# Optimization experiments

Hardware: AMD Instinct MI355X
Metric: run time of the kernel (lower is better)

Reference implementation:

```python
import jax, jax.numpy as jnp
from jax import lax
import numpy as np

D_STATE = 16
D_CONV = 4
GROUPS = 4
TOKEN = 8


def group_norm(x, w, b, groups, eps=1e-5):
    # x: [B, C, H, W]; torch GroupNorm semantics
    B, C, H, W = x.shape
    xg = x.reshape(B, groups, C // groups, H, W)
    mu = xg.mean(axis=(2, 3, 4), keepdims=True)
    var = ((xg - mu) ** 2).mean(axis=(2, 3, 4), keepdims=True)
    xg = (xg - mu) / jnp.sqrt(var + eps)
    return xg.reshape(B, C, H, W) * w[None, :, None, None] + b[None, :, None, None]


def mamba_fwd(x, in_w, conv_w, conv_b, xproj_w, dt_w, dt_b, A_log, D, out_w):
    # x: [B, L, d_model]. Faithful mamba_ssm Mamba forward (no biases on in/out proj).
    Bsz, L, _ = x.shape
    d_inner = in_w.shape[0] // 2
    dt_rank = dt_w.shape[1]
    xz = x @ in_w.T                                   # [B, L, 2*d_inner]
    xi, z = jnp.split(xz, 2, axis=-1)
    # causal depthwise conv1d (kernel D_CONV) + SiLU
    xc = lax.conv_general_dilated(
        xi.transpose(0, 2, 1), conv_w, window_strides=(1,),
        padding=[(D_CONV - 1, 0)], dimension_numbers=("NCH", "OIH", "NCH"),
        feature_group_count=d_inner)
    xc = jax.nn.silu(xc + conv_b[None, :, None]).transpose(0, 2, 1)  # [B, L, d_inner]
    xdb = xc @ xproj_w.T                               # [B, L, dt_rank + 2*d_state]
    dt, Bm, Cm = jnp.split(xdb, [dt_rank, dt_rank + D_STATE], axis=-1)
    dt = jax.nn.softplus(dt @ dt_w.T + dt_b)           # [B, L, d_inner]
    A = -jnp.exp(A_log)                                # [d_inner, d_state]
    dA = jnp.exp(dt[..., None] * A)                    # [B, L, d_inner, d_state]
    dBx = dt[..., None] * Bm[:, :, None, :] * xc[..., None]

    def step(h, inp):
        dA_t, dBx_t, C_t = inp                         # [B,di,ds],[B,di,ds],[B,ds]
        h = dA_t * h + dBx_t
        y = jnp.einsum('bds,bs->bd', h, C_t)
        return h, y

    h0 = jnp.zeros((Bsz, d_inner, D_STATE), dtype=x.dtype)
    _, ys = lax.scan(step, h0, (dA.transpose(1, 0, 2, 3),
                                dBx.transpose(1, 0, 2, 3),
                                Cm.transpose(1, 0, 2)))
    y = ys.transpose(1, 0, 2) + xc * D                 # skip term D*x
    y = y * jax.nn.silu(z)
    return y @ out_w.T


def setup_inputs() -> dict:
    key = jax.random.key(0)
    ks = iter(jax.random.split(key, 48))

    def rn(shape, s=0.02):
        return jax.random.normal(next(ks), shape, dtype=jnp.float32) * s

    B, C, H, W = 4, 64, 64, 64
    inp = {"x": jax.random.normal(next(ks), (B, C, H, W), dtype=jnp.float32)}

    def mamba_params(prefix, d_model):
        d_inner = 2 * d_model
        dt_rank = -(-d_model // 16)
        inp[prefix + "_in_w"] = rn((2 * d_inner, d_model))
        inp[prefix + "_conv_w"] = rn((d_inner, 1, D_CONV))
        inp[prefix + "_conv_b"] = rn((d_inner,))
        inp[prefix + "_xproj_w"] = rn((dt_rank + 2 * D_STATE, d_inner))
        inp[prefix + "_dt_w"] = rn((d_inner, dt_rank))
        inp[prefix + "_dt_b"] = rn((d_inner,)) + 0.5
        inp[prefix + "_A_log"] = jnp.log(jnp.tile(jnp.arange(1, D_STATE + 1, dtype=jnp.float32), (d_inner, 1)))
        inp[prefix + "_D"] = jnp.ones((d_inner,), jnp.float32)
        inp[prefix + "_out_w"] = rn((d_model, d_inner))

    mamba_params("spa", C)
    mamba_params("spe", -(-C // TOKEN))  # group_channel_num = ceil(64/8) = 8
    inp["spa_gn_w"] = jnp.ones((C,), jnp.float32)
    inp["spa_gn_b"] = jnp.zeros((C,), jnp.float32)
    inp["spe_gn_w"] = jnp.ones((C,), jnp.float32)
    inp["spe_gn_b"] = jnp.zeros((C,), jnp.float32)
    inp["att_w"] = jnp.full((2,), 0.5, jnp.float32)
    return inp


def reference(x,
              spa_in_w, spa_conv_w, spa_conv_b, spa_xproj_w, spa_dt_w, spa_dt_b,
              spa_A_log, spa_D, spa_out_w,
              spe_in_w, spe_conv_w, spe_conv_b, spe_xproj_w, spe_dt_w, spe_dt_b,
              spe_A_log, spe_D, spe_out_w,
              spa_gn_w, spa_gn_b, spe_gn_w, spe_gn_b, att_w):
    B, C, H, W = x.shape
    gcn = -(-C // TOKEN)  # C == TOKEN*gcn here, so no padding path is taken

    # --- SpaMamba: flatten all pixels into one sequence [1, B*H*W, C] ---
    xs = x.transpose(0, 2, 3, 1).reshape(1, -1, C)
    ys = mamba_fwd(xs, spa_in_w, spa_conv_w, spa_conv_b, spa_xproj_w,
                   spa_dt_w, spa_dt_b, spa_A_log, spa_D, spa_out_w)
    ys = ys.reshape(B, H, W, C).transpose(0, 3, 1, 2)
    spa = jax.nn.silu(group_norm(ys, spa_gn_w, spa_gn_b, GROUPS)) + x

    # --- SpeMamba: per-pixel spectral tokens [B*H*W, TOKEN, gcn] ---
    xe = x.transpose(0, 2, 3, 1).reshape(B * H * W, TOKEN, gcn)
    ye = mamba_fwd(xe, spe_in_w, spe_conv_w, spe_conv_b, spe_xproj_w,
                   spe_dt_w, spe_dt_b, spe_A_log, spe_D, spe_out_w)
    ye = ye.reshape(B, H, W, C).transpose(0, 3, 1, 2)
    spe = x + jax.nn.silu(group_norm(ye, spe_gn_w, spe_gn_b, GROUPS))

    w = jax.nn.softmax(att_w)
    return spa * w[0] + spe * w[1] + x
```

## Files before the change

kernel.cpp:

```cpp
#include <hip/hip_runtime.h>

__device__ __forceinline__ float siluf(float x){ return x / (1.f + __expf(-x)); }
__device__ __forceinline__ float softplusf(float x){
    return fmaxf(x, 0.f) + __logf(1.f + __expf(-fabsf(x)));
}
#if __has_builtin(__builtin_amdgcn_exp2f)
__device__ __forceinline__ float fexp2(float x){ return __builtin_amdgcn_exp2f(x); }
#else
__device__ __forceinline__ float fexp2(float x){ return exp2f(x); }
#endif

__global__ void __launch_bounds__(256) k_xpose(const float* __restrict__ x, float* __restrict__ xs){
    __shared__ float t[64][65];
    int blk = blockIdx.x;
    int b = blk >> 6;
    int hw0 = (blk & 63) << 6;
    int tid = threadIdx.x;
    if (blk == 0 && tid < 192) xs[tid] = 0.f;
    const float* xb = x + b*262144 + hw0;
    #pragma unroll
    for (int it = 0; it < 16; ++it){
        int idx = it*256 + tid;
        t[idx>>6][idx&63] = xb[(idx>>6)*4096 + (idx&63)];
    }
    __syncthreads();
    float* xsb = xs + 192 + (size_t)(b*4096 + hw0)*64;
    #pragma unroll
    for (int it = 0; it < 16; ++it){
        int idx = it*256 + tid;
        xsb[(idx>>6)*64 + (idx&63)] = t[idx&63][idx>>6];
    }
}

__global__ void __launch_bounds__(256) k_inproj_conv(const float* __restrict__ xs,
        const float* __restrict__ in_w, const float* __restrict__ cw, const float* __restrict__ cb,
        float* __restrict__ xc, float* __restrict__ zb){
    int tid = threadIdx.x;
    int l0 = blockIdx.x * 8;
    float wr[64];
    const float4* w4 = (const float4*)(in_w + tid*64);
    #pragma unroll
    for (int k = 0; k < 16; ++k){
        float4 v = w4[k];
        wr[4*k]=v.x; wr[4*k+1]=v.y; wr[4*k+2]=v.z; wr[4*k+3]=v.w;
    }
    if (tid < 128){
        float acc[11];
        #pragma unroll
        for (int r = 0; r < 11; ++r) acc[r] = 0.f;
        const float4* xr = ((const float4*)xs) + (size_t)l0*16;
        #pragma unroll
        for (int k = 0; k < 16; ++k){
            #pragma unroll
            for (int r = 0; r < 11; ++r){
                float4 v = xr[r*16 + k];
                acc[r] = fmaf(v.x, wr[4*k],   acc[r]);
                acc[r] = fmaf(v.y, wr[4*k+1], acc[r]);
                acc[r] = fmaf(v.z, wr[4*k+2], acc[r]);
                acc[r] = fmaf(v.w, wr[4*k+3], acc[r]);
            }
        }
        float cw0 = cw[tid*4+0], cw1 = cw[tid*4+1], cw2 = cw[tid*4+2], cw3 = cw[tid*4+3];
        float cbd = cb[tid];
        #pragma unroll
        for (int r = 0; r < 8; ++r){
            float a = fmaf(cw0, acc[r],   cbd);
            a = fmaf(cw1, acc[r+1], a);
            a = fmaf(cw2, acc[r+2], a);
            a = fmaf(cw3, acc[r+3], a);
            xc[(size_t)(l0+r)*128 + tid] = siluf(a);
        }
    } else {
        float acc[8];
        #pragma unroll
        for (int r = 0; r < 8; ++r) acc[r] = 0.f;
        const float4* xr = ((const float4*)(xs + 192)) + (size_t)l0*16;
        #pragma unroll
        for (int k = 0; k < 16; ++k){
            #pragma unroll
            for (int r = 0; r < 8; ++r){
                float4 v = xr[r*16 + k];
                acc[r] = fmaf(v.x, wr[4*k],   acc[r]);
                acc[r] = fmaf(v.y, wr[4*k+1], acc[r]);
                acc[r] = fmaf(v.z, wr[4*k+2], acc[r]);
                acc[r] = fmaf(v.w, wr[4*k+3], acc[r]);
            }
        }
        int dz = tid - 128;
        #pragma unroll
        for (int r = 0; r < 8; ++r) zb[(size_t)(l0+r)*128 + dz] = acc[r];
    }
}

__global__ void __launch_bounds__(256) k_scan_p1(const float* __restrict__ xc,
        const float* __restrict__ xpw, const float* __restrict__ dtw, const float* __restrict__ dtb,
        const float* __restrict__ A_log, float* __restrict__ Pb, float* __restrict__ Qb){
    __shared__ float sxc[32*128];
    __shared__ float sbm[32*16];
    __shared__ __align__(16) float dtr[32][4];
    const int tid = threadIdx.x;
    const int ch = blockIdx.x;
    {
        const float4* src = (const float4*)(xc + (size_t)ch*4096);
        float4* dst = (float4*)sxc;
        #pragma unroll
        for (int u = 0; u < 4; ++u) dst[u*256 + tid] = src[u*256 + tid];
    }
    __syncthreads();
    {
        int j = tid & 63, tg = tid >> 6;
        if (j < 20){
            const float4* w4  = (const float4*)(xpw + j*128);
            const float4* xc4 = (const float4*)sxc + tg*256;
            float acc[8];
            #pragma unroll
            for (int r = 0; r < 8; ++r) acc[r] = 0.f;
            #pragma unroll 8
            for (int k = 0; k < 32; ++k){
                float4 w = w4[k];
                #pragma unroll
                for (int r = 0; r < 8; ++r){
                    float4 v = xc4[r*32 + k];
                    acc[r] = fmaf(v.x, w.x, acc[r]);
                    acc[r] = fmaf(v.y, w.y, acc[r]);
                    acc[r] = fmaf(v.z, w.z, acc[r]);
                    acc[r] = fmaf(v.w, w.w, acc[r]);
                }
            }
            if (j < 4){
                #pragma unroll
                for (int r = 0; r < 8; ++r) dtr[tg*8+r][j] = acc[r];
            } else {
                #pragma unroll
                for (int r = 0; r < 8; ++r) sbm[(tg*8+r)*16 + (j-4)] = acc[r];
            }
        }
    }
    __syncthreads();
    const int d  = tid & 127;
    const int sh = tid >> 7;
    float A8[8];
    {
        const float4* al4 = (const float4*)(A_log + d*16 + sh*8);
        float4 v0 = al4[0], v1 = al4[1];
        A8[0]=-__expf(v0.x)*1.44269504f; A8[1]=-__expf(v0.y)*1.44269504f;
        A8[2]=-__expf(v0.z)*1.44269504f; A8[3]=-__expf(v0.w)*1.44269504f;
        A8[4]=-__expf(v1.x)*1.44269504f; A8[5]=-__expf(v1.y)*1.44269504f;
        A8[6]=-__expf(v1.z)*1.44269504f; A8[7]=-__expf(v1.w)*1.44269504f;
    }
    float4 dw = *(const float4*)(dtw + d*4);
    float dbd = dtb[d];
    float P[8], Q[8];
    #pragma unroll
    for (int s = 0; s < 8; ++s){ P[s] = 1.f; Q[s] = 0.f; }
    #pragma unroll 4
    for (int i = 0; i < 32; ++i){
        float4 dt4 = *(const float4*)dtr[i];
        float dv = dbd;
        dv = fmaf(dt4.x, dw.x, dv);
        dv = fmaf(dt4.y, dw.y, dv);
        dv = fmaf(dt4.z, dw.z, dv);
        dv = fmaf(dt4.w, dw.w, dv);
        float dt = softplusf(dv);
        float db = dt * sxc[i*128 + d];
        const float4* bmr = (const float4*)(sbm + i*16 + sh*8);
        float4 b0 = bmr[0], b1 = bmr[1];
        float bv[8] = {b0.x,b0.y,b0.z,b0.w,b1.x,b1.y,b1.z,b1.w};
        #pragma unroll
        for (int s = 0; s < 8; ++s){
            float a = fexp2(dt*A8[s]);
            P[s] *= a;
            Q[s] = fmaf(a, Q[s], db*bv[s]);
        }
    }
    float* Pp = Pb + (size_t)ch*2048 + d*16 + sh*8;
    float* Qp = Qb + (size_t)ch*2048 + d*16 + sh*8;
    ((float4*)Pp)[0] = make_float4(P[0],P[1],P[2],P[3]);
    ((float4*)Pp)[1] = make_float4(P[4],P[5],P[6],P[7]);
    ((float4*)Qp)[0] = make_float4(Q[0],Q[1],Q[2],Q[3]);
    ((float4*)Qp)[1] = make_float4(Q[4],Q[5],Q[6],Q[7]);
}

__global__ void __launch_bounds__(256) k_scan_p2a(const float* __restrict__ Pb,
        const float* __restrict__ Qb, float* __restrict__ Ps, float* __restrict__ Qs){
    int g = blockIdx.x*256 + threadIdx.x;
    int sup = g >> 11;
    int lane = g & 2047;
    float P = 1.f, Q = 0.f;
    for (int i = 0; i < 32; i += 8){
        float p[8], q[8];
        #pragma unroll
        for (int u = 0; u < 8; ++u){
            p[u] = Pb[(size_t)(sup*32+i+u)*2048 + lane];
            q[u] = Qb[(size_t)(sup*32+i+u)*2048 + lane];
        }
        #pragma unroll
        for (int u = 0; u < 8; ++u){
            P = p[u]*P;
            Q = fmaf(p[u], Q, q[u]);
        }
    }
    Ps[g] = P; Qs[g] = Q;
}

__global__ void __launch_bounds__(256) k_scan_p2c(const float* __restrict__ Pb,
        const float* __restrict__ Qb, const float* __restrict__ Ps,
        const float* __restrict__ Qs, float* __restrict__ Hs){
    int g = blockIdx.x*256 + threadIdx.x;
    int sup = g >> 11;
    int lane = g & 2047;
    float h = 0.f;
    for (int u = 0; u < sup; ++u){
        float p = Ps[u*2048 + lane];
        float q = Qs[u*2048 + lane];
        h = fmaf(p, h, q);
    }
    for (int i = 0; i < 32; i += 8){
        float p[8], q[8];
        #pragma unroll
        for (int u = 0; u < 8; ++u){
            p[u] = Pb[(size_t)(sup*32+i+u)*2048 + lane];
            q[u] = Qb[(size_t)(sup*32+i+u)*2048 + lane];
        }
        #pragma unroll
        for (int u = 0; u < 8; ++u){
            Hs[(size_t)(sup*32+i+u)*2048 + lane] = h;
            h = fmaf(p[u], h, q[u]);
        }
    }
}

__global__ void __launch_bounds__(256) k_scan_p3(const float* __restrict__ xc,
        const float* __restrict__ zb, const float* __restrict__ xpw, const float* __restrict__ dtw,
        const float* __restrict__ dtb, const float* __restrict__ A_log, const float* __restrict__ Dv,
        const float* __restrict__ Hs, float* __restrict__ yg){
    __shared__ float sxc[32*128];
    __shared__ float ypl[2][32*128];
    __shared__ float sbm[32*16];
    __shared__ float scm[32*16];
    __shared__ __align__(16) float dtr[32][4];
    const int tid = threadIdx.x;
    const int ch = blockIdx.x;
    {
        const float4* src = (const float4*)(xc + (size_t)ch*4096);
        float4* dst = (float4*)sxc;
        #pragma unroll
        for (int u = 0; u < 4; ++u) dst[u*256 + tid] = src[u*256 + tid];
    }
    __syncthreads();
    {
        int j = tid & 63, tg = tid >> 6;
        if (j < 36){
            const float4* w4  = (const float4*)(xpw + j*128);
            const float4* xc4 = (const float4*)sxc + tg*256;
            float acc[8];
            #pragma unroll
            for (int r = 0; r < 8; ++r) acc[r] = 0.f;
            #pragma unroll 8
            for (int k = 0; k < 32; ++k){
                float4 w = w4[k];
                #pragma unroll
                for (int r = 0; r < 8; ++r){
                    float4 v = xc4[r*32 + k];
                    acc[r] = fmaf(v.x, w.x, acc[r]);
                    acc[r] = fmaf(v.y, w.y, acc[r]);
                    acc[r] = fmaf(v.z, w.z, acc[r]);
                    acc[r] = fmaf(v.w, w.w, acc[r]);
                }
            }
            if (j < 4){
                #pragma unroll
                for (int r = 0; r < 8; ++r) dtr[tg*8+r][j] = acc[r];
            } else if (j < 20){
                #pragma unroll
                for (int r = 0; r < 8; ++r) sbm[(tg*8+r)*16 + (j-4)] = acc[r];
            } else {
                #pragma unroll
                for (int r = 0; r < 8; ++r) scm[(tg*8+r)*16 + (j-20)] = acc[r];
            }
        }
    }
    __syncthreads();
    const int d  = tid & 127;
    const int sh = tid >> 7;
    float A8[8], h[8];
    {
        const float4* al4 = (const float4*)(A_log + d*16 + sh*8);
        float4 v0 = al4[0], v1 = al4[1];
        A8[0]=-__expf(v0.x)*1.44269504f; A8[1]=-__expf(v0.y)*1.44269504f;
        A8[2]=-__expf(v0.z)*1.44269504f; A8[3]=-__expf(v0.w)*1.44269504f;
        A8[4]=-__expf(v1.x)*1.44269504f; A8[5]=-__expf(v1.y)*1.44269504f;
        A8[6]=-__expf(v1.z)*1.44269504f; A8[7]=-__expf(v1.w)*1.44269504f;
        const float4* h4 = (const float4*)(Hs + (size_t)ch*2048 + d*16 + sh*8);
        float4 h0 = h4[0], h1 = h4[1];
        h[0]=h0.x; h[1]=h0.y; h[2]=h0.z; h[3]=h0.w;
        h[4]=h1.x; h[5]=h1.y; h[6]=h1.z; h[7]=h1.w;
    }
    float4 dw = *(const float4*)(dtw + d*4);
    float dbd = dtb[d];
    #pragma unroll 4
    for (int i = 0; i < 32; ++i){
        float4 dt4 = *(const float4*)dtr[i];
        float dv = dbd;
        dv = fmaf(dt4.x, dw.x, dv);
        dv = fmaf(dt4.y, dw.y, dv);
        dv = fmaf(dt4.z, dw.z, dv);
        dv = fmaf(dt4.w, dw.w, dv);
        float dt = softplusf(dv);
        float db = dt * sxc[i*128 + d];
        const float4* bmr = (const float4*)(sbm + i*16 + sh*8);
        const float4* cmr = (const float4*)(scm + i*16 + sh*8);
        float4 b0 = bmr[0], b1 = bmr[1];
        float4 c0 = cmr[0], c1 = cmr[1];
        float bv[8] = {b0.x,b0.y,b0.z,b0.w,b1.x,b1.y,b1.z,b1.w};
        float cv[8] = {c0.x,c0.y,c0.z,c0.w,c1.x,c1.y,c1.z,c1.w};
        float yp = 0.f;
        #pragma unroll
        for (int s = 0; s < 8; ++s){
            float a = fexp2(dt*A8[s]);
            h[s] = fmaf(a, h[s], db*bv[s]);
            yp = fmaf(h[s], cv[s], yp);
        }
        ypl[sh][i*128 + d] = yp;
    }
    __syncthreads();
    #pragma unroll
    for (int it = 0; it < 16; ++it){
        int idx = it*256 + tid;
        int i = idx >> 7, dd = idx & 127;
        float yp = ypl[0][i*128+dd] + ypl[1][i*128+dd];
        float xcd = sxc[i*128+dd];
        float zv = zb[(size_t)ch*4096 + idx];
        yg[(size_t)ch*4096 + idx] = (yp + xcd*Dv[dd]) * siluf(zv);
    }
}

__global__ void __launch_bounds__(256) k_spa_outproj(const float* __restrict__ yg,
        const float* __restrict__ ow, float* __restrict__ ys, float* __restrict__ sp){
    __shared__ float part[16][64];
    __shared__ float pg[2][2][4];
    int tid = threadIdx.x;
    int c  = tid & 63;
    int kh = (tid >> 6) & 1;
    int rg = tid >> 7;
    int l0 = blockIdx.x*16 + rg*8;
    float wr[64];
    const float4* w4 = (const float4*)(ow + c*128 + kh*64);
    #pragma unroll
    for (int k = 0; k < 16; ++k){
        float4 v = w4[k];
        wr[4*k]=v.x; wr[4*k+1]=v.y; wr[4*k+2]=v.z; wr[4*k+3]=v.w;
    }
    float acc[8];
    #pragma unroll
    for (int r = 0; r < 8; ++r) acc[r] = 0.f;
    const float4* yr = (const float4*)(yg + (size_t)l0*128 + kh*64);
    #pragma unroll
    for (int k = 0; k < 16; ++k){
        #pragma unroll
        for (int r = 0; r < 8; ++r){
            float4 v = yr[r*32 + k];
            acc[r] = fmaf(v.x, wr[4*k],   acc[r]);
            acc[r] = fmaf(v.y, wr[4*k+1], acc[r]);
            acc[r] = fmaf(v.z, wr[4*k+2], acc[r]);
            acc[r] = fmaf(v.w, wr[4*k+3], acc[r]);
        }
    }
    if (kh == 1){
        #pragma unroll
        for (int r = 0; r < 8; ++r) part[rg*8+r][c] = acc[r];
    }
    __syncthreads();
    if (kh == 0){
        float s = 0.f, ss = 0.f;
        #pragma unroll
        for (int r = 0; r < 8; ++r){
            float v = acc[r] + part[rg*8+r][c];
            ys[(size_t)(l0+r)*64 + c] = v;
            s += v; ss += v*v;
        }
        s += __shfl_xor(s,1); ss += __shfl_xor(ss,1);
        s += __shfl_xor(s,2); ss += __shfl_xor(ss,2);
        s += __shfl_xor(s,4); ss += __shfl_xor(ss,4);
        s += __shfl_xor(s,8); ss += __shfl_xor(ss,8);
        if ((c & 15) == 0){ pg[0][rg][c>>4] = s; pg[1][rg][c>>4] = ss; }
    }
    __syncthreads();
    if (tid < 4){
        int b = blockIdx.x >> 8, blk = blockIdx.x & 255;
        float S  = pg[0][0][tid] + pg[0][1][tid];
        float SS = pg[1][0][tid] + pg[1][1][tid];
        float* dst = sp + (size_t)(((0*4 + b)*4 + tid)*256 + blk)*2;
        dst[0] = S; dst[1] = SS;
    }
}

__global__ void __launch_bounds__(256) k_spe(
        const float* __restrict__ x,
        const float* __restrict__ in_w, const float* __restrict__ cw, const float* __restrict__ cb,
        const float* __restrict__ xpw, const float* __restrict__ dtw, const float* __restrict__ dtb,
        const float* __restrict__ A_log, const float* __restrict__ Dv, const float* __restrict__ ow,
        float* __restrict__ ye, float* __restrict__ sp)
{
    __shared__ float xe[64][17];
    __shared__ float xcl[8][16][17];
    __shared__ float bml[8][16][17];
    __shared__ float cml[8][16][17];
    __shared__ float dtl[8][17];
    __shared__ float yl[8][16][17];
    __shared__ float spg[2][4][4];

    const int tid = threadIdx.x;
    const int pix = tid >> 4;
    const int d   = tid & 15;
    const int p0  = blockIdx.x * 16;
    const int b   = p0 >> 12;
    const int hw0 = p0 & 4095;

    const float* xb = x + b*262144 + hw0;
    #pragma unroll
    for (int it = 0; it < 4; ++it){
        int idx = it*256 + tid;
        xe[idx>>4][idx&15] = xb[(idx>>4)*4096 + (idx&15)];
    }
    __syncthreads();

    float wi[8], wz[8];
    #pragma unroll
    for (int g = 0; g < 8; ++g){ wi[g] = in_w[d*8+g]; wz[g] = in_w[(16+d)*8+g]; }
    float xi[8], zz[8];
    #pragma unroll
    for (int t = 0; t < 8; ++t){
        float ai = 0.f, az = 0.f;
        #pragma unroll
        for (int g = 0; g < 8; ++g){
            float v = xe[t*8+g][pix];
            ai = fmaf(v, wi[g], ai);
            az = fmaf(v, wz[g], az);
        }
        xi[t] = ai; zz[t] = az;
    }
    float c0 = cw[d*4+0], c1 = cw[d*4+1], c2 = cw[d*4+2], c3 = cw[d*4+3];
    float cbd = cb[d];
    float xcr[8];
    #pragma unroll
    for (int t = 0; t < 8; ++t){
        float a = fmaf(c3, xi[t], cbd);
        if (t >= 1) a = fmaf(c2, xi[t-1], a);
        if (t >= 2) a = fmaf(c1, xi[t-2], a);
        if (t >= 3) a = fmaf(c0, xi[t-3], a);
        xcr[t] = siluf(a);
        xcl[t][d][pix] = xcr[t];
    }
    __syncthreads();

    {
        const float* wr = xpw + d*16;
        #pragma unroll
        for (int t = 0; t < 8; ++t){
            float acc = 0.f;
            #pragma unroll
            for (int k = 0; k < 16; ++k) acc = fmaf(xcl[t][k][pix], wr[k], acc);
            if (d == 0) dtl[t][pix] = acc;
            else bml[t][d-1][pix] = acc;
        }
    }
    {
        const float* wr = xpw + (17+d)*16;
        #pragma unroll
        for (int t = 0; t < 8; ++t){
            float acc = 0.f;
            #pragma unroll
            for (int k = 0; k < 16; ++k) acc = fmaf(xcl[t][k][pix], wr[k], acc);
            cml[t][d][pix] = acc;
        }
    }
    if (d == 15){
        const float* wr = xpw + 16*16;
        #pragma unroll
        for (int t = 0; t < 8; ++t){
            float acc = 0.f;
            #pragma unroll
            for (int k = 0; k < 16; ++k) acc = fmaf(xcl[t][k][pix], wr[k], acc);
            bml[t][15][pix] = acc;
        }
    }
    __syncthreads();

    float A16[16];
    #pragma unroll
    for (int s = 0; s < 16; ++s) A16[s] = -__expf(A_log[d*16+s]) * 1.44269504f;
    float dwd = dtw[d], dbd = dtb[d], Dd = Dv[d];
    float h[16];
    #pragma unroll
    for (int s = 0; s < 16; ++s) h[s] = 0.f;
    #pragma unroll
    for (int t = 0; t < 8; ++t){
        float dtd = softplusf(fmaf(dtl[t][pix], dwd, dbd));
        float db = dtd * xcr[t];
        float yp = 0.f;
        #pragma unroll
        for (int s = 0; s < 16; ++s){
            float a = fexp2(dtd*A16[s]);
            h[s] = fmaf(a, h[s], db*bml[t][s][pix]);
            yp = fmaf(h[s], cml[t][s][pix], yp);
        }
        yl[t][d][pix] = (yp + xcr[t]*Dd) * siluf(zz[t]);
    }
    __syncthreads();

    int t = d >> 1, m0 = (d & 1)*4;
    float acc[4];
    #pragma unroll
    for (int mm = 0; mm < 4; ++mm){
        const float* wr = ow + (m0+mm)*16;
        float a = 0.f;
        #pragma unroll
        for (int k = 0; k < 16; ++k) a = fmaf(yl[t][k][pix], wr[k], a);
        acc[mm] = a;
    }
    float4 o; o.x=acc[0]; o.y=acc[1]; o.z=acc[2]; o.w=acc[3];
    *(float4*)(ye + (size_t)(p0+pix)*64 + t*8 + m0) = o;

    float s  = acc[0]+acc[1]+acc[2]+acc[3];
    float ss = acc[0]*acc[0]+acc[1]*acc[1]+acc[2]*acc[2]+acc[3]*acc[3];
    s += __shfl_xor(s,1);  ss += __shfl_xor(ss,1);
    s += __shfl_xor(s,2);  ss += __shfl_xor(ss,2);
    s += __shfl_xor(s,16); ss += __shfl_xor(ss,16);
    s += __shfl_xor(s,32); ss += __shfl_xor(ss,32);
    int lane = tid & 63, wv = tid >> 6;
    if ((lane & 51) == 0){ spg[0][wv][(lane>>2)&3] = s; spg[1][wv][(lane>>2)&3] = ss; }
    __syncthreads();
    if (tid < 4){
        int blk = blockIdx.x & 255;
        float S  = spg[0][0][tid]+spg[0][1][tid]+spg[0][2][tid]+spg[0][3][tid];
        float SS = spg[1][0][tid]+spg[1][1][tid]+spg[1][2][tid]+spg[1][3][tid];
        float* dst = sp + (size_t)(((1*4 + b)*4 + tid)*256 + blk)*2;
        dst[0] = S; dst[1] = SS;
    }
}

__global__ void __launch_bounds__(256) k_final(const float* __restrict__ x,
        const float* __restrict__ ys, const float* __restrict__ ye,
        const float* __restrict__ sp,
        const float* __restrict__ gsw, const float* __restrict__ gsb,
        const float* __restrict__ gew, const float* __restrict__ geb,
        const float* __restrict__ attw, float* __restrict__ out){
    __shared__ float st[16];
    __shared__ float tys[32][65];
    __shared__ float tye[32][65];
    int tid = threadIdx.x;
    int b   = blockIdx.x >> 7;
    int hw0 = (blockIdx.x & 127) << 5;
    {
        int combo = tid >> 5;
        int j = tid & 31;
        int t = combo >> 2, g = combo & 3;
        const float4* bp = (const float4*)(sp + (size_t)((t*4+b)*4 + g)*512 + j*16);
        float s = 0.f, ss = 0.f;
        #pragma unroll
        for (int k = 0; k < 4; ++k){ float4 v = bp[k]; s += v.x+v.z; ss += v.y+v.w; }
        s += __shfl_xor(s,1);  ss += __shfl_xor(ss,1);
        s += __shfl_xor(s,2);  ss += __shfl_xor(ss,2);
        s += __shfl_xor(s,4);  ss += __shfl_xor(ss,4);
        s += __shfl_xor(s,8);  ss += __shfl_xor(ss,8);
        s += __shfl_xor(s,16); ss += __shfl_xor(ss,16);
        if (j == 0){
            float m = s * (1.f/65536.f);
            float v = ss * (1.f/65536.f) - m*m;
            st[combo*2]   = m;
            st[combo*2+1] = rsqrtf(v + 1e-5f);
        }
    }
    const float* ysb = ys + ((size_t)(b*4096 + hw0))*64;
    const float* yeb = ye + ((size_t)(b*4096 + hw0))*64;
    #pragma unroll
    for (int it = 0; it < 8; ++it){
        int idx = it*256 + tid;
        tys[idx>>6][idx&63] = ysb[idx];
        tye[idx>>6][idx&63] = yeb[idx];
    }
    __syncthreads();
    float a0 = attw[0], a1 = attw[1];
    float mx = fmaxf(a0, a1);
    float e0 = __expf(a0-mx), e1 = __expf(a1-mx);
    float inv = 1.f/(e0+e1);
    float w0 = e0*inv, w1 = e1*inv;
    #pragma unroll
    for (int it = 0; it < 8; ++it){
        int idx = it*256 + tid;
        int c = idx >> 5, hwi = idx & 31;
        int g = c >> 4;
        size_t gx = ((size_t)(b*64 + c))*4096 + hw0 + hwi;
        float xv = x[gx];
        float ns = (tys[hwi][c] - st[g*2])     * st[g*2+1]     * gsw[c] + gsb[c];
        float ne = (tye[hwi][c] - st[8+g*2])   * st[8+g*2+1]   * gew[c] + geb[c];
        out[gx] = w0*(siluf(ns)+xv) + w1*(xv+siluf(ne)) + xv;
    }
}

#define OFF_XS 0u
#define OFF_XC 1048832u
#define OFF_Z  3145984u
#define OFF_PB 5243136u
#define OFF_QB 6291712u
#define OFF_YG 7340288u
#define OFF_HS 9437440u
#define OFF_PS 10486016u
#define OFF_QS 10518784u
#define OFF_SP 10551552u

extern "C" void kernel_launch(void* const* d_in, const int* in_sizes, int n_in,
                              void* d_out, int out_size, void* d_ws, size_t ws_size,
                              hipStream_t stream) {
    const float* x           = (const float*)d_in[0];
    const float* spa_in_w    = (const float*)d_in[1];
    const float* spa_conv_w  = (const float*)d_in[2];
    const float* spa_conv_b  = (const float*)d_in[3];
    const float* spa_xproj_w = (const float*)d_in[4];
    const float* spa_dt_w    = (const float*)d_in[5];
    const float* spa_dt_b    = (const float*)d_in[6];
    const float* spa_A_log   = (const float*)d_in[7];
    const float* spa_D       = (const float*)d_in[8];
    const float* spa_out_w   = (const float*)d_in[9];
    const float* spe_in_w    = (const float*)d_in[10];
    const float* spe_conv_w  = (const float*)d_in[11];
    const float* spe_conv_b  = (const float*)d_in[12];
    const float* spe_xproj_w = (const float*)d_in[13];
    const float* spe_dt_w    = (const float*)d_in[14];
    const float* spe_dt_b    = (const float*)d_in[15];
    const float* spe_A_log   = (const float*)d_in[16];
    const float* spe_D       = (const float*)d_in[17];
    const float* spe_out_w   = (const float*)d_in[18];
    const float* spa_gn_w    = (const float*)d_in[19];
    const float* spa_gn_b    = (const float*)d_in[20];
    const float* spe_gn_w    = (const float*)d_in[21];
    const float* spe_gn_b    = (const float*)d_in[22];
    const float* att_w       = (const float*)d_in[23];

    float* ws  = (float*)d_ws;
    float* xs  = ws + OFF_XS;
    float* xc  = ws + OFF_XC;
    float* zb  = ws + OFF_Z;
    float* Pb  = ws + OFF_PB;
    float* Qb  = ws + OFF_QB;
    float* yg  = ws + OFF_YG;
    float* Hs  = ws + OFF_HS;
    float* Ps  = ws + OFF_PS;
    float* Qs  = ws + OFF_QS;
    float* sp  = ws + OFF_SP;
    float* ysb = ws + OFF_XS;
    float* yeb = ws + OFF_Z;
    float* out = (float*)d_out;

    k_xpose      <<<256,  256, 0, stream>>>(x, xs);
    k_inproj_conv<<<2048, 256, 0, stream>>>(xs, spa_in_w, spa_conv_w, spa_conv_b, xc, zb);
    k_scan_p1    <<<512,  256, 0, stream>>>(xc, spa_xproj_w, spa_dt_w, spa_dt_b, spa_A_log, Pb, Qb);
    k_scan_p2a   <<<128,  256, 0, stream>>>(Pb, Qb, Ps, Qs);
    k_scan_p2c   <<<128,  256, 0, stream>>>(Pb, Qb, Ps, Qs, Hs);
    k_scan_p3    <<<512,  256, 0, stream>>>(xc, zb, spa_xproj_w, spa_dt_w, spa_dt_b,
                                            spa_A_log, spa_D, Hs, yg);
    k_spa_outproj<<<1024, 256, 0, stream>>>(yg, spa_out_w, ysb, sp);
    k_spe        <<<1024, 256, 0, stream>>>(x, spe_in_w, spe_conv_w, spe_conv_b, spe_xproj_w,
                                            spe_dt_w, spe_dt_b, spe_A_log, spe_D, spe_out_w,
                                            yeb, sp);
    k_final      <<<512,  256, 0, stream>>>(x, ysb, yeb, sp, spa_gn_w, spa_gn_b,
                                            spe_gn_w, spe_gn_b, att_w, out);
}
```

Baseline: 141.4 us.

## Fuse spa out-proj into scan p3 and co-schedule spectral Mamba with scan p1

The spectral Mamba branch now runs as extra blocks (512..1535) inside the spatial scan phase-1 kernel, so the two independent workloads share one launch and can fill the GPU together. The spatial output projection and its group-norm partial sums move into the tail of scan_p3, which reuses the gated y held in shared memory instead of writing yg to global memory and reading it back in a separate kernel. This removes two launches and one full intermediate round trip. In exchange the fused p1 kernel needs about 40 KB of shared memory per block and p3 carries more register pressure (a 64-float weight array plus 16 accumulators), which may lower occupancy. The workspace layout and the partial-sum indexing in k_final are adjusted to match.

After: 120.2 us. 1.18x faster.

```diff
diff --git a/kernel.cpp b/kernel.cpp
--- a/kernel.cpp
+++ b/kernel.cpp
@@ -92,93 +92,239 @@
     }
 }
 
-__global__ void __launch_bounds__(256) k_scan_p1(const float* __restrict__ xc,
-        const float* __restrict__ xpw, const float* __restrict__ dtw, const float* __restrict__ dtb,
-        const float* __restrict__ A_log, float* __restrict__ Pb, float* __restrict__ Qb){
-    __shared__ float sxc[32*128];
-    __shared__ float sbm[32*16];
-    __shared__ __align__(16) float dtr[32][4];
+__global__ void __launch_bounds__(256) k_p1_spe(
+        const float* __restrict__ xc, const float* __restrict__ xpw, const float* __restrict__ dtw,
+        const float* __restrict__ dtb, const float* __restrict__ A_log,
+        float* __restrict__ Pb, float* __restrict__ Qb,
+        const float* __restrict__ x,
+        const float* __restrict__ ein_w, const float* __restrict__ ecw, const float* __restrict__ ecb,
+        const float* __restrict__ expw, const float* __restrict__ edtw, const float* __restrict__ edtb,
+        const float* __restrict__ eA_log, const float* __restrict__ eDv, const float* __restrict__ eow,
+        float* __restrict__ ye, float* __restrict__ sp)
+{
+    __shared__ float smem[9960];
     const int tid = threadIdx.x;
-    const int ch = blockIdx.x;
-    {
-        const float4* src = (const float4*)(xc + (size_t)ch*4096);
-        float4* dst = (float4*)sxc;
-        #pragma unroll
-        for (int u = 0; u < 4; ++u) dst[u*256 + tid] = src[u*256 + tid];
-    }
-    __syncthreads();
-    {
-        int j = tid & 63, tg = tid >> 6;
-        if (j < 20){
-            const float4* w4  = (const float4*)(xpw + j*128);
-            const float4* xc4 = (const float4*)sxc + tg*256;
-            float acc[8];
-            #pragma unroll
-            for (int r = 0; r < 8; ++r) acc[r] = 0.f;
-            #pragma unroll 8
-            for (int k = 0; k < 32; ++k){
-                float4 w = w4[k];
-                #pragma unroll
-                for (int r = 0; r < 8; ++r){
-                    float4 v = xc4[r*32 + k];
-                    acc[r] = fmaf(v.x, w.x, acc[r]);
-                    acc[r] = fmaf(v.y, w.y, acc[r]);
-                    acc[r] = fmaf(v.z, w.z, acc[r]);
-                    acc[r] = fmaf(v.w, w.w, acc[r]);
+    if (blockIdx.x < 512){
+        float* sxc = smem;
+        float* sbm = smem + 4096;
+        float* dtr = smem + 4608;
+        const int ch = blockIdx.x;
+        {
+            const float4* src = (const float4*)(xc + (size_t)ch*4096);
+            float4* dst = (float4*)sxc;
+            #pragma unroll
+            for (int u = 0; u < 4; ++u) dst[u*256 + tid] = src[u*256 + tid];
+        }
+        __syncthreads();
+        {
+            int j = tid & 63, tg = tid >> 6;
+            if (j < 20){
+                const float4* w4  = (const float4*)(xpw + j*128);
+                const float4* xc4 = (const float4*)sxc + tg*256;
+                float acc[8];
+                #pragma unroll
+                for (int r = 0; r < 8; ++r) acc[r] = 0.f;
+                #pragma unroll 8
+                for (int k = 0; k < 32; ++k){
+                    float4 w = w4[k];
+                    #pragma unroll
+                    for (int r = 0; r < 8; ++r){
+                        float4 v = xc4[r*32 + k];
+                        acc[r] = fmaf(v.x, w.x, acc[r]);
+                        acc[r] = fmaf(v.y, w.y, acc[r]);
+                        acc[r] = fmaf(v.z, w.z, acc[r]);
+                        acc[r] = fmaf(v.w, w.w, acc[r]);
+                    }
                 }
-            }
-            if (j < 4){
-                #pragma unroll
-                for (int r = 0; r < 8; ++r) dtr[tg*8+r][j] = acc[r];
-            } else {
-                #pragma unroll
-                for (int r = 0; r < 8; ++r) sbm[(tg*8+r)*16 + (j-4)] = acc[r];
-            }
-        }
-    }
-    __syncthreads();
-    const int d  = tid & 127;
-    const int sh = tid >> 7;
-    float A8[8];
-    {
-        const float4* al4 = (const float4*)(A_log + d*16 + sh*8);
-        float4 v0 = al4[0], v1 = al4[1];
-        A8[0]=-__expf(v0.x)*1.44269504f; A8[1]=-__expf(v0.y)*1.44269504f;
-        A8[2]=-__expf(v0.z)*1.44269504f; A8[3]=-__expf(v0.w)*1.44269504f;
-        A8[4]=-__expf(v1.x)*1.44269504f; A8[5]=-__expf(v1.y)*1.44269504f;
-        A8[6]=-__expf(v1.z)*1.44269504f; A8[7]=-__expf(v1.w)*1.44269504f;
-    }
-    float4 dw = *(const float4*)(dtw + d*4);
-    float dbd = dtb[d];
-    float P[8], Q[8];
-    #pragma unroll
-    for (int s = 0; s < 8; ++s){ P[s] = 1.f; Q[s] = 0.f; }
-    #pragma unroll 4
-    for (int i = 0; i < 32; ++i){
-        float4 dt4 = *(const float4*)dtr[i];
-        float dv = dbd;
-        dv = fmaf(dt4.x, dw.x, dv);
-        dv = fmaf(dt4.y, dw.y, dv);
-        dv = fmaf(dt4.z, dw.z, dv);
-        dv = fmaf(dt4.w, dw.w, dv);
-        float dt = softplusf(dv);
-        float db = dt * sxc[i*128 + d];
-        const float4* bmr = (const float4*)(sbm + i*16 + sh*8);
-        float4 b0 = bmr[0], b1 = bmr[1];
-        float bv[8] = {b0.x,b0.y,b0.z,b0.w,b1.x,b1.y,b1.z,b1.w};
-        #pragma unroll
-        for (int s = 0; s < 8; ++s){
-            float a = fexp2(dt*A8[s]);
-            P[s] *= a;
-            Q[s] = fmaf(a, Q[s], db*bv[s]);
-        }
-    }
-    float* Pp = Pb + (size_t)ch*2048 + d*16 + sh*8;
-    float* Qp = Qb + (size_t)ch*2048 + d*16 + sh*8;
-    ((float4*)Pp)[0] = make_float4(P[0],P[1],P[2],P[3]);
-    ((float4*)Pp)[1] = make_float4(P[4],P[5],P[6],P[7]);
-    ((float4*)Qp)[0] = make_float4(Q[0],Q[1],Q[2],Q[3]);
-    ((float4*)Qp)[1] = make_float4(Q[4],Q[5],Q[6],Q[7]);
+                if (j < 4){
+                    #pragma unroll
+                    for (int r = 0; r < 8; ++r) dtr[(tg*8+r)*4 + j] = acc[r];
+                } else {
+                    #pragma unroll
+                    for (int r = 0; r < 8; ++r) sbm[(tg*8+r)*16 + (j-4)] = acc[r];
+                }
+            }
+        }
+        __syncthreads();
+        const int d  = tid & 127;
+        const int sh = tid >> 7;
+        float A8[8];
+        {
+            const float4* al4 = (const float4*)(A_log + d*16 + sh*8);
+            float4 v0 = al4[0], v1 = al4[1];
+            A8[0]=-__expf(v0.x)*1.44269504f; A8[1]=-__expf(v0.y)*1.44269504f;
+            A8[2]=-__expf(v0.z)*1.44269504f; A8[3]=-__expf(v0.w)*1.44269504f;
+            A8[4]=-__expf(v1.x)*1.44269504f; A8[5]=-__expf(v1.y)*1.44269504f;
+            A8[6]=-__expf(v1.z)*1.44269504f; A8[7]=-__expf(v1.w)*1.44269504f;
+        }
+        float4 dw = *(const float4*)(dtw + d*4);
+        float dbd = dtb[d];
+        float P[8], Q[8];
+        #pragma unroll
+        for (int s = 0; s < 8; ++s){ P[s] = 1.f; Q[s] = 0.f; }
+        #pragma unroll 4
+        for (int i = 0; i < 32; ++i){
+            float4 dt4 = *(const float4*)(dtr + i*4);
+            float dv = dbd;
+            dv = fmaf(dt4.x, dw.x, dv);
+            dv = fmaf(dt4.y, dw.y, dv);
+            dv = fmaf(dt4.z, dw.z, dv);
+            dv = fmaf(dt4.w, dw.w, dv);
+            float dt = softplusf(dv);
+            float db = dt * sxc[i*128 + d];
+            const float4* bmr = (const float4*)(sbm + i*16 + sh*8);
+            float4 b0 = bmr[0], b1 = bmr[1];
+            float bv[8] = {b0.x,b0.y,b0.z,b0.w,b1.x,b1.y,b1.z,b1.w};
+            #pragma unroll
+            for (int s = 0; s < 8; ++s){
+                float a = fexp2(dt*A8[s]);
+                P[s] *= a;
+                Q[s] = fmaf(a, Q[s], db*bv[s]);
+            }
+        }
+        float* Pp = Pb + (size_t)ch*2048 + d*16 + sh*8;
+        float* Qp = Qb + (size_t)ch*2048 + d*16 + sh*8;
+        ((float4*)Pp)[0] = make_float4(P[0],P[1],P[2],P[3]);
+        ((float4*)Pp)[1] = make_float4(P[4],P[5],P[6],P[7]);
+        ((float4*)Qp)[0] = make_float4(Q[0],Q[1],Q[2],Q[3]);
+        ((float4*)Qp)[1] = make_float4(Q[4],Q[5],Q[6],Q[7]);
+    } else {
+        float* xe  = smem;
+        float* xcl = smem + 1088;
+        float* bml = smem + 3264;
+        float* cml = smem + 5440;
+        float* dtl = smem + 7616;
+        float* yl  = smem + 7752;
+        float* spg = smem + 9928;
+        const int pix = tid >> 4;
+        const int d   = tid & 15;
+        const int eb  = blockIdx.x - 512;
+        const int p0  = eb * 16;
+        const int b   = p0 >> 12;
+        const int hw0 = p0 & 4095;
+
+        const float* xb = x + b*262144 + hw0;
+        #pragma unroll
+        for (int it = 0; it < 4; ++it){
+            int idx = it*256 + tid;
+            xe[(idx>>4)*17 + (idx&15)] = xb[(idx>>4)*4096 + (idx&15)];
+        }
+        __syncthreads();
+
+        float wi[8], wz[8];
+        #pragma unroll
+        for (int g = 0; g < 8; ++g){ wi[g] = ein_w[d*8+g]; wz[g] = ein_w[(16+d)*8+g]; }
+        float xi[8], zz[8];
+        #pragma unroll
+        for (int t = 0; t < 8; ++t){
+            float ai = 0.f, az = 0.f;
+            #pragma unroll
+            for (int g = 0; g < 8; ++g){
+                float v = xe[(t*8+g)*17 + pix];
+                ai = fmaf(v, wi[g], ai);
+                az = fmaf(v, wz[g], az);
+            }
+            xi[t] = ai; zz[t] = az;
+        }
+        float c0 = ecw[d*4+0], c1 = ecw[d*4+1], c2 = ecw[d*4+2], c3 = ecw[d*4+3];
+        float cbd = ecb[d];
+        float xcr[8];
+        #pragma unroll
+        for (int t = 0; t < 8; ++t){
+            float a = fmaf(c3, xi[t], cbd);
+            if (t >= 1) a = fmaf(c2, xi[t-1], a);
+            if (t >= 2) a = fmaf(c1, xi[t-2], a);
+            if (t >= 3) a = fmaf(c0, xi[t-3], a);
+            xcr[t] = siluf(a);
+            xcl[(t*16+d)*17 + pix] = xcr[t];
+        }
+        __syncthreads();
+
+        {
+            const float* wr = expw + d*16;
+            #pragma unroll
+            for (int t = 0; t < 8; ++t){
+                float acc = 0.f;
+                #pragma unroll
+                for (int k = 0; k < 16; ++k) acc = fmaf(xcl[(t*16+k)*17 + pix], wr[k], acc);
+                if (d == 0) dtl[t*17 + pix] = acc;
+                else bml[(t*16+d-1)*17 + pix] = acc;
+            }
+        }
+        {
+            const float* wr = expw + (17+d)*16;
+            #pragma unroll
+            for (int t = 0; t < 8; ++t){
+                float acc = 0.f;
+                #pragma unroll
+                for (int k = 0; k < 16; ++k) acc = fmaf(xcl[(t*16+k)*17 + pix], wr[k], acc);
+                cml[(t*16+d)*17 + pix] = acc;
+            }
+        }
+        if (d == 15){
+            const float* wr = expw + 16*16;
+            #pragma unroll
+            for (int t = 0; t < 8; ++t){
+                float acc = 0.f;
+                #pragma unroll
+                for (int k = 0; k < 16; ++k) acc = fmaf(xcl[(t*16+k)*17 + pix], wr[k], acc);
+                bml[(t*16+15)*17 + pix] = acc;
+            }
+        }
+        __syncthreads();
+
+        float A16[16];
+        #pragma unroll
+        for (int s = 0; s < 16; ++s) A16[s] = -__expf(eA_log[d*16+s]) * 1.44269504f;
+        float dwd = edtw[d], dbd = edtb[d], Dd = eDv[d];
+        float h[16];
+        #pragma unroll
+        for (int s = 0; s < 16; ++s) h[s] = 0.f;
+        #pragma unroll
+        for (int t = 0; t < 8; ++t){
+            float dtd = softplusf(fmaf(dtl[t*17 + pix], dwd, dbd));
+            float db = dtd * xcr[t];
+            float yp = 0.f;
+            #pragma unroll
+            for (int s = 0; s < 16; ++s){
+                float a = fexp2(dtd*A16[s]);
+                h[s] = fmaf(a, h[s], db*bml[(t*16+s)*17 + pix]);
+                yp = fmaf(h[s], cml[(t*16+s)*17 + pix], yp);
+            }
+            yl[(t*16+d)*17 + pix] = (yp + xcr[t]*Dd) * siluf(zz[t]);
+        }
+        __syncthreads();
+
+        int t = d >> 1, m0 = (d & 1)*4;
+        float acc[4];
+        #pragma unroll
+        for (int mm = 0; mm < 4; ++mm){
+            const float* wr = eow + (m0+mm)*16;
+            float a = 0.f;
+            #pragma unroll
+            for (int k = 0; k < 16; ++k) a = fmaf(yl[(t*16+k)*17 + pix], wr[k], a);
+            acc[mm] = a;
+        }
+        float4 o; o.x=acc[0]; o.y=acc[1]; o.z=acc[2]; o.w=acc[3];
+        *(float4*)(ye + (size_t)(p0+pix)*64 + t*8 + m0) = o;
+
+        float s  = acc[0]+acc[1]+acc[2]+acc[3];
+        float ss = acc[0]*acc[0]+acc[1]*acc[1]+acc[2]*acc[2]+acc[3]*acc[3];
+        s += __shfl_xor(s,1);  ss += __shfl_xor(ss,1);
+        s += __shfl_xor(s,2);  ss += __shfl_xor(ss,2);
+        s += __shfl_xor(s,16); ss += __shfl_xor(ss,16);
+        s += __shfl_xor(s,32); ss += __shfl_xor(ss,32);
+        int lane = tid & 63, wv = tid >> 6;
+        if ((lane & 51) == 0){ spg[0*16 + wv*4 + ((lane>>2)&3)] = s; spg[16 + wv*4 + ((lane>>2)&3)] = ss; }
+        __syncthreads();
+        if (tid < 4){
+            int blk = eb & 255;
+            float S  = spg[0*16+0*4+tid]+spg[0*16+1*4+tid]+spg[0*16+2*4+tid]+spg[0*16+3*4+tid];
+            float SS = spg[16+0*4+tid]+spg[16+1*4+tid]+spg[16+2*4+tid]+spg[16+3*4+tid];
+            float* dst = sp + (size_t)(((4 + b)*4 + tid)*512 + blk*2);
+            dst[0] = S; dst[1] = SS;
+        }
+    }
 }
 
 __global__ void __launch_bounds__(256) k_scan_p2a(const float* __restrict__ Pb,
@@ -233,12 +379,14 @@
 __global__ void __launch_bounds__(256) k_scan_p3(const float* __restrict__ xc,
         const float* __restrict__ zb, const float* __restrict__ xpw, const float* __restrict__ dtw,
         const float* __restrict__ dtb, const float* __restrict__ A_log, const float* __restrict__ Dv,
-        const float* __restrict__ Hs, float* __restrict__ yg){
+        const float* __restrict__ Hs, const float* __restrict__ ow,
+        float* __restrict__ ys, float* __restrict__ sp){
     __shared__ float sxc[32*128];
     __shared__ float ypl[2][32*128];
     __shared__ float sbm[32*16];
     __shared__ float scm[32*16];
     __shared__ __align__(16) float dtr[32][4];
+    __shared__ float pgs[2][2][4];
     const int tid = threadIdx.x;
     const int ch = blockIdx.x;
     {
@@ -327,216 +475,66 @@
     #pragma unroll
     for (int it = 0; it < 16; ++it){
         int idx = it*256 + tid;
-        int i = idx >> 7, dd = idx & 127;
-        float yp = ypl[0][i*128+dd] + ypl[1][i*128+dd];
-        float xcd = sxc[i*128+dd];
+        float yp = ypl[0][idx] + ypl[1][idx];
+        float xcd = sxc[idx];
         float zv = zb[(size_t)ch*4096 + idx];
-        yg[(size_t)ch*4096 + idx] = (yp + xcd*Dv[dd]) * siluf(zv);
-    }
-}
-
-__global__ void __launch_bounds__(256) k_spa_outproj(const float* __restrict__ yg,
-        const float* __restrict__ ow, float* __restrict__ ys, float* __restrict__ sp){
-    __shared__ float part[16][64];
-    __shared__ float pg[2][2][4];
-    int tid = threadIdx.x;
-    int c  = tid & 63;
-    int kh = (tid >> 6) & 1;
-    int rg = tid >> 7;
-    int l0 = blockIdx.x*16 + rg*8;
-    float wr[64];
-    const float4* w4 = (const float4*)(ow + c*128 + kh*64);
-    #pragma unroll
-    for (int k = 0; k < 16; ++k){
-        float4 v = w4[k];
-        wr[4*k]=v.x; wr[4*k+1]=v.y; wr[4*k+2]=v.z; wr[4*k+3]=v.w;
-    }
-    float acc[8];
-    #pragma unroll
-    for (int r = 0; r < 8; ++r) acc[r] = 0.f;
-    const float4* yr = (const float4*)(yg + (size_t)l0*128 + kh*64);
-    #pragma unroll
-    for (int k = 0; k < 16; ++k){
-        #pragma unroll
-        for (int r = 0; r < 8; ++r){
-            float4 v = yr[r*32 + k];
-            acc[r] = fmaf(v.x, wr[4*k],   acc[r]);
-            acc[r] = fmaf(v.y, wr[4*k+1], acc[r]);
-            acc[r] = fmaf(v.z, wr[4*k+2], acc[r]);
-            acc[r] = fmaf(v.w, wr[4*k+3], acc[r]);
-        }
-    }
-    if (kh == 1){
-        #pragma unroll
-        for (int r = 0; r < 8; ++r) part[rg*8+r][c] = acc[r];
+        ypl[0][idx] = (yp + xcd*Dv[idx & 127]) * siluf(zv);
     }
     __syncthreads();
-    if (kh == 0){
-        float s = 0.f, ss = 0.f;
-        #pragma unroll
-        for (int r = 0; r < 8; ++r){
-            float v = acc[r] + part[rg*8+r][c];
-            ys[(size_t)(l0+r)*64 + c] = v;
-            s += v; ss += v*v;
-        }
-        s += __shfl_xor(s,1); ss += __shfl_xor(ss,1);
-        s += __shfl_xor(s,2); ss += __shfl_xor(ss,2);
-        s += __shfl_xor(s,4); ss += __shfl_xor(ss,4);
-        s += __shfl_xor(s,8); ss += __shfl_xor(ss,8);
-        if ((c & 15) == 0){ pg[0][rg][c>>4] = s; pg[1][rg][c>>4] = ss; }
-    }
-    __syncthreads();
-    if (tid < 4){
-        int b = blockIdx.x >> 8, blk = blockIdx.x & 255;
-        float S  = pg[0][0][tid] + pg[0][1][tid];
-        float SS = pg[1][0][tid] + pg[1][1][tid];
-        float* dst = sp + (size_t)(((0*4 + b)*4 + tid)*256 + blk)*2;
-        dst[0] = S; dst[1] = SS;
-    }
-}
-
-__global__ void __launch_bounds__(256) k_spe(
-        const float* __restrict__ x,
-        const float* __restrict__ in_w, const float* __restrict__ cw, const float* __restrict__ cb,
-        const float* __restrict__ xpw, const float* __restrict__ dtw, const float* __restrict__ dtb,
-        const float* __restrict__ A_log, const float* __restrict__ Dv, const float* __restrict__ ow,
-        float* __restrict__ ye, float* __restrict__ sp)
-{
-    __shared__ float xe[64][17];
-    __shared__ float xcl[8][16][17];
-    __shared__ float bml[8][16][17];
-    __shared__ float cml[8][16][17];
-    __shared__ float dtl[8][17];
-    __shared__ float yl[8][16][17];
-    __shared__ float spg[2][4][4];
-
-    const int tid = threadIdx.x;
-    const int pix = tid >> 4;
-    const int d   = tid & 15;
-    const int p0  = blockIdx.x * 16;
-    const int b   = p0 >> 12;
-    const int hw0 = p0 & 4095;
-
-    const float* xb = x + b*262144 + hw0;
-    #pragma unroll
-    for (int it = 0; it < 4; ++it){
-        int idx = it*256 + tid;
-        xe[idx>>4][idx&15] = xb[(idx>>4)*4096 + (idx&15)];
-    }
-    __syncthreads();
-
-    float wi[8], wz[8];
-    #pragma unroll
-    for (int g = 0; g < 8; ++g){ wi[g] = in_w[d*8+g]; wz[g] = in_w[(16+d)*8+g]; }
-    float xi[8], zz[8];
-    #pragma unroll
-    for (int t = 0; t < 8; ++t){
-        float ai = 0.f, az = 0.f;
-        #pragma unroll
-        for (int g = 0; g < 8; ++g){
-            float v = xe[t*8+g][pix];
-            ai = fmaf(v, wi[g], ai);
-            az = fmaf(v, wz[g], az);
-        }
-        xi[t] = ai; zz[t] = az;
-    }
-    float c0 = cw[d*4+0], c1 = cw[d*4+1], c2 = cw[d*4+2], c3 = cw[d*4+3];
-    float cbd = cb[d];
-    float xcr[8];
-    #pragma unroll
-    for (int t = 0; t < 8; ++t){
-        float a = fmaf(c3, xi[t], cbd);
-        if (t >= 1) a = fmaf(c2, xi[t-1], a);
-        if (t >= 2) a = fmaf(c1, xi[t-2], a);
-        if (t >= 3) a = fmaf(c0, xi[t-3], a);
-        xcr[t] = siluf(a);
-        xcl[t][d][pix] = xcr[t];
-    }
-    __syncthreads();
-
     {
-        const float* wr = xpw + d*16;
-        #pragma unroll
-        for (int t = 0; t < 8; ++t){
-            float acc = 0.f;
-            #pragma unroll
-            for (int k = 0; k < 16; ++k) acc = fmaf(xcl[t][k][pix], wr[k], acc);
-            if (d == 0) dtl[t][pix] = acc;
-            else bml[t][d-1][pix] = acc;
-        }
-    }
-    {
-        const float* wr = xpw + (17+d)*16;
-        #pragma unroll
-        for (int t = 0; t < 8; ++t){
-            float acc = 0.f;
-            #pragma unroll
-            for (int k = 0; k < 16; ++k) acc = fmaf(xcl[t][k][pix], wr[k], acc);
-            cml[t][d][pix] = acc;
-        }
-    }
-    if (d == 15){
-        const float* wr = xpw + 16*16;
-        #pragma unroll
-        for (int t = 0; t < 8; ++t){
-            float acc = 0.f;
-            #pragma unroll
-            for (int k = 0; k < 16; ++k) acc = fmaf(xcl[t][k][pix], wr[k], acc);
-            bml[t][15][pix] = acc;
-        }
-    }
-    __syncthreads();
-
-    float A16[16];
-    #pragma unroll
-    for (int s = 0; s < 16; ++s) A16[s] = -__expf(A_log[d*16+s]) * 1.44269504f;
-    float dwd = dtw[d], dbd = dtb[d], Dd = Dv[d];
-    float h[16];
-    #pragma unroll
-    for (int s = 0; s < 16; ++s) h[s] = 0.f;
-    #pragma unroll
-    for (int t = 0; t < 8; ++t){
-        float dtd = softplusf(fmaf(dtl[t][pix], dwd, dbd));
-        float db = dtd * xcr[t];
-        float yp = 0.f;
-        #pragma unroll
-        for (int s = 0; s < 16; ++s){
-            float a = fexp2(dtd*A16[s]);
-            h[s] = fmaf(a, h[s], db*bml[t][s][pix]);
-            yp = fmaf(h[s], cml[t][s][pix], yp);
-        }
-        yl[t][d][pix] = (yp + xcr[t]*Dd) * siluf(zz[t]);
-    }
-    __syncthreads();
-
-    int t = d >> 1, m0 = (d & 1)*4;
-    float acc[4];
-    #pragma unroll
-    for (int mm = 0; mm < 4; ++mm){
-        const float* wr = ow + (m0+mm)*16;
-        float a = 0.f;
-        #pragma unroll
-        for (int k = 0; k < 16; ++k) a = fmaf(yl[t][k][pix], wr[k], a);
-        acc[mm] = a;
-    }
-    float4 o; o.x=acc[0]; o.y=acc[1]; o.z=acc[2]; o.w=acc[3];
-    *(float4*)(ye + (size_t)(p0+pix)*64 + t*8 + m0) = o;
-
-    float s  = acc[0]+acc[1]+acc[2]+acc[3];
-    float ss = acc[0]*acc[0]+acc[1]*acc[1]+acc[2]*acc[2]+acc[3]*acc[3];
-    s += __shfl_xor(s,1);  ss += __shfl_xor(ss,1);
-    s += __shfl_xor(s,2);  ss += __shfl_xor(ss,2);
-    s += __shfl_xor(s,16); ss += __shfl_xor(ss,16);
-    s += __shfl_xor(s,32); ss += __shfl_xor(ss,32);
-    int lane = tid & 63, wv = tid >> 6;
-    if ((lane & 51) == 0){ spg[0][wv][(lane>>2)&3] = s; spg[1][wv][(lane>>2)&3] = ss; }
-    __syncthreads();
-    if (tid < 4){
-        int blk = blockIdx.x & 255;
-        float S  = spg[0][0][tid]+spg[0][1][tid]+spg[0][2][tid]+spg[0][3][tid];
-        float SS = spg[1][0][tid]+spg[1][1][tid]+spg[1][2][tid]+spg[1][3][tid];
-        float* dst = sp + (size_t)(((1*4 + b)*4 + tid)*256 + blk)*2;
-        dst[0] = S; dst[1] = SS;
+        int c  = tid & 63;
+        int kh = (tid >> 6) & 1;
+        int rg = tid >> 7;
+        float wr[64];
+        const float4* w4o = (const float4*)(ow + c*128 + kh*64);
+        #pragma unroll
+        for (int k = 0; k < 16; ++k){
+            float4 v = w4o[k];
+            wr[4*k]=v.x; wr[4*k+1]=v.y; wr[4*k+2]=v.z; wr[4*k+3]=v.w;
+        }
+        float acc[16];
+        #pragma unroll
+        for (int r = 0; r < 16; ++r) acc[r] = 0.f;
+        const float4* y4 = (const float4*)(ypl[0] + rg*16*128 + kh*64);
+        #pragma unroll
+        for (int k = 0; k < 16; ++k){
+            #pragma unroll
+            for (int r = 0; r < 16; ++r){
+                float4 v = y4[r*32 + k];
+                acc[r] = fmaf(v.x, wr[4*k],   acc[r]);
+                acc[r] = fmaf(v.y, wr[4*k+1], acc[r]);
+                acc[r] = fmaf(v.z, wr[4*k+2], acc[r]);
+                acc[r] = fmaf(v.w, wr[4*k+3], acc[r]);
+            }
+        }
+        float* part = ypl[1];
+        if (kh == 1){
+            #pragma unroll
+            for (int r = 0; r < 16; ++r) part[(rg*16+r)*64 + c] = acc[r];
+        }
+        __syncthreads();
+        if (kh == 0){
+            float s = 0.f, ss = 0.f;
+            #pragma unroll
+            for (int r = 0; r < 16; ++r){
+                float v = acc[r] + part[(rg*16+r)*64 + c];
+                ys[(size_t)(ch*32 + rg*16 + r)*64 + c] = v;
+                s += v; ss += v*v;
+            }
+            s += __shfl_xor(s,1); ss += __shfl_xor(ss,1);
+            s += __shfl_xor(s,2); ss += __shfl_xor(ss,2);
+            s += __shfl_xor(s,4); ss += __shfl_xor(ss,4);
+            s += __shfl_xor(s,8); ss += __shfl_xor(ss,8);
+            if ((c & 15) == 0){ pgs[0][rg][c>>4] = s; pgs[1][rg][c>>4] = ss; }
+        }
+        __syncthreads();
+        if (tid < 4){
+            int b = ch >> 7, blk = ch & 127;
+            float S  = pgs[0][0][tid] + pgs[0][1][tid];
+            float SS = pgs[1][0][tid] + pgs[1][1][tid];
+            float* dst = sp + (size_t)((b*4 + tid)*512 + blk*2);
+            dst[0] = S; dst[1] = SS;
+        }
     }
 }
 
@@ -556,10 +554,16 @@
         int combo = tid >> 5;
         int j = tid & 31;
         int t = combo >> 2, g = combo & 3;
-        const float4* bp = (const float4*)(sp + (size_t)((t*4+b)*4 + g)*512 + j*16);
         float s = 0.f, ss = 0.f;
-        #pragma unroll
-        for (int k = 0; k < 4; ++k){ float4 v = bp[k]; s += v.x+v.z; ss += v.y+v.w; }
+        if (t == 0){
+            const float4* bp = (const float4*)(sp + (size_t)(b*4 + g)*512 + j*8);
+            #pragma unroll
+            for (int k = 0; k < 2; ++k){ float4 v = bp[k]; s += v.x+v.z; ss += v.y+v.w; }
+        } else {
+            const float4* bp = (const float4*)(sp + (size_t)((4+b)*4 + g)*512 + j*16);
+            #pragma unroll
+            for (int k = 0; k < 4; ++k){ float4 v = bp[k]; s += v.x+v.z; ss += v.y+v.w; }
+        }
         s += __shfl_xor(s,1);  ss += __shfl_xor(ss,1);
         s += __shfl_xor(s,2);  ss += __shfl_xor(ss,2);
         s += __shfl_xor(s,4);  ss += __shfl_xor(ss,4);
@@ -604,11 +608,11 @@
 #define OFF_Z  3145984u
 #define OFF_PB 5243136u
 #define OFF_QB 6291712u
-#define OFF_YG 7340288u
-#define OFF_HS 9437440u
-#define OFF_PS 10486016u
-#define OFF_QS 10518784u
-#define OFF_SP 10551552u
+#define OFF_HS 7340288u
+#define OFF_YE 8388864u
+#define OFF_PS 9437440u
+#define OFF_QS 9470208u
+#define OFF_SP 9502976u
 
 extern "C" void kernel_launch(void* const* d_in, const int* in_sizes, int n_in,
                               void* d_out, int out_size, void* d_ws, size_t ws_size,
@@ -644,26 +648,25 @@
     float* zb  = ws + OFF_Z;
     float* Pb  = ws + OFF_PB;
     float* Qb  = ws + OFF_QB;
-    float* yg  = ws + OFF_YG;
     float* Hs  = ws + OFF_HS;
     float* Ps  = ws + OFF_PS;
     float* Qs  = ws + OFF_QS;
     float* sp  = ws + OFF_SP;
     float* ysb = ws + OFF_XS;
-    float* yeb = ws + OFF_Z;
+    float* yeb = ws + OFF_YE;
     float* out = (float*)d_out;
 
     k_xpose      <<<256,  256, 0, stream>>>(x, xs);
     k_inproj_conv<<<2048, 256, 0, stream>>>(xs, spa_in_w, spa_conv_w, spa_conv_b, xc, zb);
-    k_scan_p1    <<<512,  256, 0, stream>>>(xc, spa_xproj_w, spa_dt_w, spa_dt_b, spa_A_log, Pb, Qb);
+    k_p1_spe     <<<1536, 256, 0, stream>>>(xc, spa_xproj_w, spa_dt_w, spa_dt_b, spa_A_log,
+                                            Pb, Qb,
+                                            x, spe_in_w, spe_conv_w, spe_conv_b, spe_xproj_w,
+                                            spe_dt_w, spe_dt_b, spe_A_log, spe_D, spe_out_w,
+                                            yeb, sp);
     k_scan_p2a   <<<128,  256, 0, stream>>>(Pb, Qb, Ps, Qs);
     k_scan_p2c   <<<128,  256, 0, stream>>>(Pb, Qb, Ps, Qs, Hs);
     k_scan_p3    <<<512,  256, 0, stream>>>(xc, zb, spa_xproj_w, spa_dt_w, spa_dt_b,
-                                            spa_A_log, spa_D, Hs, yg);
-    k_spa_outproj<<<1024, 256, 0, stream>>>(yg, spa_out_w, ysb, sp);
-    k_spe        <<<1024, 256, 0, stream>>>(x, spe_in_w, spe_conv_w, spe_conv_b, spe_xproj_w,
-                                            spe_dt_w, spe_dt_b, spe_A_log, spe_D, spe_out_w,
-                                            yeb, sp);
+                                            spa_A_log, spa_D, Hs, spa_out_w, ysb, sp);
     k_final      <<<512,  256, 0, stream>>>(x, ysb, yeb, sp, spa_gn_w, spa_gn_b,
                                             spe_gn_w, spe_gn_b, att_w, out);
 }
```
